# Performance work log

Hardware: AMD Instinct MI355X
Metric: run time of the kernel (lower is better)

The kernel has to match this reference:

```python
import jax, jax.numpy as jnp
import numpy as np

EPS = 1e-9


def _pairwise_sqdist(x1, x2):
    # x1: (B,n,3), x2: (B,m,3) -> (B,n,m) squared euclidean distances
    s1 = jnp.sum(x1 * x1, axis=-1)
    s2 = jnp.sum(x2 * x2, axis=-1)
    cross = jnp.einsum('bnd,bmd->bnm', x1, x2)
    return jnp.maximum(s1[:, :, None] + s2[:, None, :] - 2.0 * cross, 0.0)


def _approxmatch(x1, x2):
    # Faithful port of the approxmatch CUDA kernel (Fan et al. EMD approx).
    B, n, _ = x1.shape
    m = x2.shape[1]
    if n >= m:
        multiL, multiR = 1.0, float(n // m)   # integer division as in CUDA
    else:
        multiL, multiR = float(m // n), 1.0
    dist = _pairwise_sqdist(x1, x2)  # (B,n,m)
    # j = 7 .. -1 -> level = -4^j ; j = -2 -> level = 0  (10 sweeps total)
    levels = jnp.concatenate([
        -(4.0 ** jnp.arange(7, -2, -1, dtype=jnp.float32)),
        jnp.zeros((1,), jnp.float32)])
    match0 = jnp.zeros((B, n, m), jnp.float32)
    remainL0 = jnp.full((B, n), multiL, jnp.float32)
    remainR0 = jnp.full((B, m), multiR, jnp.float32)

    def body(carry, level):
        match, remainL, remainR = carry
        e = jnp.exp(level * dist)                              # (B,n,m)
        suml = EPS + jnp.einsum('bnm,bm->bn', e, remainR)
        ratioL = remainL / suml                                # (B,n)
        sumr = remainR * jnp.einsum('bnm,bn->bm', e, ratioL)   # (B,m)
        consumption = jnp.minimum(remainR / (sumr + EPS), 1.0)
        ratioR = consumption * remainR                         # (B,m)
        remainR = jnp.maximum(0.0, remainR - sumr)
        w = e * ratioL[:, :, None] * ratioR[:, None, :]        # flow k->l
        match = match + w
        remainL = jnp.maximum(0.0, remainL - jnp.sum(w, axis=-1))
        return (match, remainL, remainR), None

    (match, _, _), _ = jax.lax.scan(body, (match0, remainL0, remainR0), levels)
    return match, dist


def setup_inputs() -> dict:
    key = jax.random.key(0)
    k1, k2 = jax.random.split(key)
    B, N = 4, 4096
    xyz1 = jax.random.normal(k1, (B, 3, N), dtype=jnp.float32)
    xyz2 = jax.random.normal(k2, (B, 3, N), dtype=jnp.float32)
    return {"xyz1": xyz1, "xyz2": xyz2}


def reference(xyz1, xyz2):
    # transpose=True: BCN -> BNC
    x1 = jnp.transpose(xyz1, (0, 2, 1))
    x2 = jnp.transpose(xyz2, (0, 2, 1))
    match, dist = _approxmatch(x1, x2)
    d = jnp.sqrt(jnp.maximum(dist, 1e-20))
    cost = jnp.sum(match * d, axis=(1, 2))            # (B,)
    emd = cost / min(x1.shape[1], x2.shape[1])
    return jnp.mean(emd)                               # reduce_mean=True
```

## Files before the change

kernel.cpp:

```cpp
#include <hip/hip_runtime.h>


#define NPTS 4096
#define BATCH 4
#define EMD_EPS 1e-9f
#define TILE 1024
#define RPW 4
#define THREADS 256
#define RPB 16
#define NBLK (NPTS / RPB)

__device__ __forceinline__ float fexp2(float x) {
#if __has_builtin(__builtin_amdgcn_exp2f)
    return __builtin_amdgcn_exp2f(x);
#else
    return exp2f(x);
#endif
}
__device__ __forceinline__ float fsqrt(float x) {
#if __has_builtin(__builtin_amdgcn_sqrtf)
    return __builtin_amdgcn_sqrtf(x);
#else
    return __sqrtf(x);
#endif
}

__device__ __forceinline__ float wave_reduce(float v) {
    v += __shfl_xor(v, 32);
    v += __shfl_xor(v, 16);
    v += __shfl_xor(v, 8);
    v += __shfl_xor(v, 4);
    v += __shfl_xor(v, 2);
    v += __shfl_xor(v, 1);
    return v;
}

__global__ void k_init(float* __restrict__ remainL, float* __restrict__ remainR,
                       float* __restrict__ cost_part) {
    int i = blockIdx.x * blockDim.x + threadIdx.x;
    if (i < BATCH * NPTS) {
        remainL[i] = 1.0f;
        remainR[i] = 1.0f;
    }
    if (i < BATCH * NBLK) cost_part[i] = 0.0f;
}

__global__ __launch_bounds__(THREADS, 2) void k_ratioL0(
        const float* __restrict__ xyz1, const float* __restrict__ xyz2,
        float* __restrict__ ratioL, float ls2) {
    const int b = blockIdx.y;
    const int tid = threadIdx.x;
    const int wave = tid >> 6;
    const int lane = tid & 63;
    const int row0 = blockIdx.x * RPB + wave * RPW;

    const float* x1 = xyz1 + b * 3 * NPTS;
    const float* x2 = xyz2 + b * 3 * NPTS;
    const float2* x2x = (const float2*)(x2);
    const float2* x2y = (const float2*)(x2 + NPTS);
    const float2* x2z = (const float2*)(x2 + 2 * NPTS);

    float px[RPW], py[RPW], pz[RPW];
    float2 acc[RPW];
#pragma unroll
    for (int r = 0; r < RPW; ++r) {
        px[r] = x1[row0 + r];
        py[r] = x1[NPTS + row0 + r];
        pz[r] = x1[2 * NPTS + row0 + r];
        acc[r] = make_float2(0.0f, 0.0f);
    }
    __shared__ float4 sA[TILE / 2];
    __shared__ float2 sZ[TILE / 2];

    for (int c0 = 0; c0 < NPTS; c0 += TILE) {
        __syncthreads();
        for (int i = tid; i < TILE / 2; i += THREADS) {
            int e = c0 / 2 + i;
            float2 xx = x2x[e], yy = x2y[e];
            sA[i] = make_float4(xx.x, xx.y, yy.x, yy.y);
            sZ[i] = x2z[e];
        }
        __syncthreads();
#pragma unroll 2
        for (int j = 0; j < TILE / 128; ++j) {
            float4 a = sA[lane + 64 * j];
            float2 z = sZ[lane + 64 * j];
#pragma unroll
            for (int r = 0; r < RPW; ++r) {
                float dx0 = px[r] - a.x, dx1 = px[r] - a.y;
                float dy0 = py[r] - a.z, dy1 = py[r] - a.w;
                float dz0 = pz[r] - z.x, dz1 = pz[r] - z.y;
                float d0 = fmaf(dx0, dx0, fmaf(dy0, dy0, dz0 * dz0));
                float d1 = fmaf(dx1, dx1, fmaf(dy1, dy1, dz1 * dz1));
                acc[r].x += fexp2(ls2 * d0);
                acc[r].y += fexp2(ls2 * d1);
            }
        }
    }
#pragma unroll
    for (int r = 0; r < RPW; ++r) {
        float s = wave_reduce(acc[r].x + acc[r].y);
        if (lane == 0)
            ratioL[b * NPTS + row0 + r] = 1.0f / (EMD_EPS + s);
    }
}

__global__ __launch_bounds__(THREADS, 2) void k_ratioR(
        const float* __restrict__ xyz1, const float* __restrict__ xyz2,
        const float* __restrict__ ratioL, float* __restrict__ ratioR,
        float* __restrict__ remainR, float ls2) {
    const int b = blockIdx.y;
    const int tid = threadIdx.x;
    const int wave = tid >> 6;
    const int lane = tid & 63;
    const int col0 = blockIdx.x * RPB + wave * RPW;

    const float* x1 = xyz1 + b * 3 * NPTS;
    const float* x2 = xyz2 + b * 3 * NPTS;
    const float2* x1x = (const float2*)(x1);
    const float2* x1y = (const float2*)(x1 + NPTS);
    const float2* x1z = (const float2*)(x1 + 2 * NPTS);
    const float2* wLv = (const float2*)(ratioL + b * NPTS);

    float px[RPW], py[RPW], pz[RPW];
    float2 acc[RPW];
#pragma unroll
    for (int r = 0; r < RPW; ++r) {
        px[r] = x2[col0 + r];
        py[r] = x2[NPTS + col0 + r];
        pz[r] = x2[2 * NPTS + col0 + r];
        acc[r] = make_float2(0.0f, 0.0f);
    }
    __shared__ float4 sA[TILE / 2];
    __shared__ float4 sB[TILE / 2];

    for (int c0 = 0; c0 < NPTS; c0 += TILE) {
        __syncthreads();
        for (int i = tid; i < TILE / 2; i += THREADS) {
            int e = c0 / 2 + i;
            float2 xx = x1x[e], yy = x1y[e], zz = x1z[e], ww = wLv[e];
            sA[i] = make_float4(xx.x, xx.y, yy.x, yy.y);
            sB[i] = make_float4(zz.x, zz.y, ww.x, ww.y);
        }
        __syncthreads();
#pragma unroll 2
        for (int j = 0; j < TILE / 128; ++j) {
            float4 a = sA[lane + 64 * j];
            float4 bq = sB[lane + 64 * j];
#pragma unroll
            for (int r = 0; r < RPW; ++r) {
                float dx0 = px[r] - a.x, dx1 = px[r] - a.y;
                float dy0 = py[r] - a.z, dy1 = py[r] - a.w;
                float dz0 = pz[r] - bq.x, dz1 = pz[r] - bq.y;
                float d0 = fmaf(dx0, dx0, fmaf(dy0, dy0, dz0 * dz0));
                float d1 = fmaf(dx1, dx1, fmaf(dy1, dy1, dz1 * dz1));
                acc[r].x = fmaf(fexp2(ls2 * d0), bq.z, acc[r].x);
                acc[r].y = fmaf(fexp2(ls2 * d1), bq.w, acc[r].y);
            }
        }
    }
#pragma unroll
    for (int r = 0; r < RPW; ++r) {
        float s = wave_reduce(acc[r].x + acc[r].y);
        if (lane == 0) {
            int idx = b * NPTS + col0 + r;
            float rv = remainR[idx];
            float sumr = rv * s;
            float cons = fminf(rv / (sumr + EMD_EPS), 1.0f);
            ratioR[idx] = cons * rv;
            remainR[idx] = fmaxf(0.0f, rv - sumr);
        }
    }
}

template <bool SQ>
__global__ __launch_bounds__(THREADS, 2) void k_cost_fused(
        const float* __restrict__ xyz1, const float* __restrict__ xyz2,
        float* __restrict__ ratioL, const float* __restrict__ ratioR,
        float* __restrict__ remainL, const float* __restrict__ remainR,
        float* __restrict__ cost_part, float ls2, float ls2n) {
    const int b = blockIdx.y;
    const int tid = threadIdx.x;
    const int wave = tid >> 6;
    const int lane = tid & 63;
    const int row0 = blockIdx.x * RPB + wave * RPW;

    const float* x1 = xyz1 + b * 3 * NPTS;
    const float* x2 = xyz2 + b * 3 * NPTS;
    const float2* x2x = (const float2*)(x2);
    const float2* x2y = (const float2*)(x2 + NPTS);
    const float2* x2z = (const float2*)(x2 + 2 * NPTS);
    const float2* wRv = (const float2*)(ratioR + b * NPTS);
    const float2* w2v = (const float2*)(remainR + b * NPTS);

    float px[RPW], py[RPW], pz[RPW];
    float2 acc_a[RPW], acc_c[RPW], acc_s[RPW];
#pragma unroll
    for (int r = 0; r < RPW; ++r) {
        px[r] = x1[row0 + r];
        py[r] = x1[NPTS + row0 + r];
        pz[r] = x1[2 * NPTS + row0 + r];
        acc_a[r] = make_float2(0.0f, 0.0f);
        acc_c[r] = make_float2(0.0f, 0.0f);
        acc_s[r] = make_float2(0.0f, 0.0f);
    }
    __shared__ float4 sA[TILE / 2];
    __shared__ float4 sB[TILE / 2];
    __shared__ float2 sC[TILE / 2];
    __shared__ float s_cost[THREADS / 64];

    for (int c0 = 0; c0 < NPTS; c0 += TILE) {
        __syncthreads();
        for (int i = tid; i < TILE / 2; i += THREADS) {
            int e = c0 / 2 + i;
            float2 xx = x2x[e], yy = x2y[e], zz = x2z[e], wr = wRv[e];
            sA[i] = make_float4(xx.x, xx.y, yy.x, yy.y);
            sB[i] = make_float4(zz.x, zz.y, wr.x, wr.y);
            sC[i] = w2v[e];
        }
        __syncthreads();
#pragma unroll 2
        for (int j = 0; j < TILE / 128; ++j) {
            float4 a = sA[lane + 64 * j];
            float4 bq = sB[lane + 64 * j];
            float2 c = sC[lane + 64 * j];
#pragma unroll
            for (int r = 0; r < RPW; ++r) {
                float dx0 = px[r] - a.x, dx1 = px[r] - a.y;
                float dy0 = py[r] - a.z, dy1 = py[r] - a.w;
                float dz0 = pz[r] - bq.x, dz1 = pz[r] - bq.y;
                float d0 = fmaf(dx0, dx0, fmaf(dy0, dy0, dz0 * dz0));
                float d1 = fmaf(dx1, dx1, fmaf(dy1, dy1, dz1 * dz1));
                float er0, er1;
                if (SQ) {
                    float e20 = fexp2(ls2n * d0);
                    float e21 = fexp2(ls2n * d1);
                    acc_s[r].x = fmaf(e20, c.x, acc_s[r].x);
                    acc_s[r].y = fmaf(e21, c.y, acc_s[r].y);
                    float e40 = e20 * e20, e41 = e21 * e21;
                    er0 = (e40 * e40) * bq.z;
                    er1 = (e41 * e41) * bq.w;
                } else {
                    er0 = fexp2(ls2 * d0) * bq.z;
                    er1 = fexp2(ls2 * d1) * bq.w;
                    acc_s[r].x += c.x;
                    acc_s[r].y += c.y;
                }
                acc_a[r].x += er0;
                acc_a[r].y += er1;
                acc_c[r].x = fmaf(er0, fsqrt(d0), acc_c[r].x);
                acc_c[r].y = fmaf(er1, fsqrt(d1), acc_c[r].y);
            }
        }
    }
    float wcost = 0.0f;
#pragma unroll
    for (int r = 0; r < RPW; ++r) {
        float sa = wave_reduce(acc_a[r].x + acc_a[r].y);
        float sc = wave_reduce(acc_c[r].x + acc_c[r].y);
        float ss = wave_reduce(acc_s[r].x + acc_s[r].y);
        if (lane == 0) {
            int idx = b * NPTS + row0 + r;
            float rl = ratioL[idx];
            float rem = fmaxf(0.0f, remainL[idx] - rl * sa);
            remainL[idx] = rem;
            ratioL[idx] = rem / (EMD_EPS + ss);
            wcost = fmaf(rl, sc, wcost);
        }
    }
    if (lane == 0) s_cost[wave] = wcost;
    __syncthreads();
    if (tid == 0) {
        float t = s_cost[0] + s_cost[1] + s_cost[2] + s_cost[3];
        cost_part[b * NBLK + blockIdx.x] += t;
    }
}

__global__ void k_sum_ratioL(const float* __restrict__ ratioL, float* __restrict__ S_L) {
    const int b = blockIdx.x;
    const int tid = threadIdx.x;
    float s = 0.0f;
    for (int i = tid; i < NPTS; i += 256) s += ratioL[b * NPTS + i];
    s = wave_reduce(s);
    __shared__ float sw[4];
    if ((tid & 63) == 0) sw[tid >> 6] = s;
    __syncthreads();
    if (tid == 0) S_L[b] = sw[0] + sw[1] + sw[2] + sw[3];
}

__global__ void k_ratioR_l0(const float* __restrict__ remainR,
                            const float* __restrict__ S_L,
                            float* __restrict__ ratioR) {
    int i = blockIdx.x * blockDim.x + threadIdx.x;
    int b = i >> 12;
    float rv = remainR[i];
    float sumr = rv * S_L[b];
    float cons = fminf(rv / (sumr + EMD_EPS), 1.0f);
    ratioR[i] = cons * rv;
}

__global__ __launch_bounds__(THREADS, 2) void k_cost_l0(
        const float* __restrict__ xyz1, const float* __restrict__ xyz2,
        const float* __restrict__ ratioL, const float* __restrict__ ratioR,
        float* __restrict__ cost_part) {
    const int b = blockIdx.y;
    const int tid = threadIdx.x;
    const int wave = tid >> 6;
    const int lane = tid & 63;
    const int row0 = blockIdx.x * RPB + wave * RPW;

    const float* x1 = xyz1 + b * 3 * NPTS;
    const float* x2 = xyz2 + b * 3 * NPTS;
    const float2* x2x = (const float2*)(x2);
    const float2* x2y = (const float2*)(x2 + NPTS);
    const float2* x2z = (const float2*)(x2 + 2 * NPTS);
    const float2* wRv = (const float2*)(ratioR + b * NPTS);

    float px[RPW], py[RPW], pz[RPW];
    float2 acc_c[RPW];
#pragma unroll
    for (int r = 0; r < RPW; ++r) {
        px[r] = x1[row0 + r];
        py[r] = x1[NPTS + row0 + r];
        pz[r] = x1[2 * NPTS + row0 + r];
        acc_c[r] = make_float2(0.0f, 0.0f);
    }
    __shared__ float4 sA[TILE / 2];
    __shared__ float4 sB[TILE / 2];
    __shared__ float s_cost[THREADS / 64];

    for (int c0 = 0; c0 < NPTS; c0 += TILE) {
        __syncthreads();
        for (int i = tid; i < TILE / 2; i += THREADS) {
            int e = c0 / 2 + i;
            float2 xx = x2x[e], yy = x2y[e], zz = x2z[e], wr = wRv[e];
            sA[i] = make_float4(xx.x, xx.y, yy.x, yy.y);
            sB[i] = make_float4(zz.x, zz.y, wr.x, wr.y);
        }
        __syncthreads();
#pragma unroll 2
        for (int j = 0; j < TILE / 128; ++j) {
            float4 a = sA[lane + 64 * j];
            float4 bq = sB[lane + 64 * j];
#pragma unroll
            for (int r = 0; r < RPW; ++r) {
                float dx0 = px[r] - a.x, dx1 = px[r] - a.y;
                float dy0 = py[r] - a.z, dy1 = py[r] - a.w;
                float dz0 = pz[r] - bq.x, dz1 = pz[r] - bq.y;
                float d0 = fmaf(dx0, dx0, fmaf(dy0, dy0, dz0 * dz0));
                float d1 = fmaf(dx1, dx1, fmaf(dy1, dy1, dz1 * dz1));
                acc_c[r].x = fmaf(bq.z, fsqrt(d0), acc_c[r].x);
                acc_c[r].y = fmaf(bq.w, fsqrt(d1), acc_c[r].y);
            }
        }
    }
    float wcost = 0.0f;
#pragma unroll
    for (int r = 0; r < RPW; ++r) {
        float sc = wave_reduce(acc_c[r].x + acc_c[r].y);
        if (lane == 0)
            wcost = fmaf(ratioL[b * NPTS + row0 + r], sc, wcost);
    }
    if (lane == 0) s_cost[wave] = wcost;
    __syncthreads();
    if (tid == 0) {
        float t = s_cost[0] + s_cost[1] + s_cost[2] + s_cost[3];
        cost_part[b * NBLK + blockIdx.x] += t;
    }
}

__global__ void k_final(const float* __restrict__ cost_part, float* __restrict__ out) {
    const int tid = threadIdx.x;
    float s = 0.0f;
    for (int i = tid; i < BATCH * NBLK; i += 256) s += cost_part[i];
    s = wave_reduce(s);
    __shared__ float sw[4];
    if ((tid & 63) == 0) sw[tid >> 6] = s;
    __syncthreads();
    if (tid == 0) out[0] = (sw[0] + sw[1] + sw[2] + sw[3]) / ((float)NPTS * (float)BATCH);
}

extern "C" void kernel_launch(void* const* d_in, const int* in_sizes, int n_in,
                              void* d_out, int out_size, void* d_ws, size_t ws_size,
                              hipStream_t stream) {
    const float* xyz1 = (const float*)d_in[0];
    const float* xyz2 = (const float*)d_in[1];
    float* out = (float*)d_out;

    float* ws = (float*)d_ws;
    float* remainL  = ws;
    float* remainR  = ws + 1 * BATCH * NPTS;
    float* ratioL   = ws + 2 * BATCH * NPTS;
    float* ratioR   = ws + 3 * BATCH * NPTS;
    float* cost_part = ws + 4 * BATCH * NPTS;
    float* S_L      = cost_part + BATCH * NBLK;

    static const float levels[10] = {
        -16384.0f, -4096.0f, -1024.0f, -256.0f, -64.0f,
        -16.0f, -4.0f, -1.0f, -0.25f, 0.0f};
    float ls2[10];
    for (int t = 0; t < 10; ++t)
        ls2[t] = (float)(levels[t] * 1.4426950408889634);

    dim3 grid(NBLK, BATCH);

    k_init<<<(BATCH * NPTS + 255) / 256, 256, 0, stream>>>(remainL, remainR, cost_part);
    k_ratioL0<<<grid, THREADS, 0, stream>>>(xyz1, xyz2, ratioL, ls2[0]);
    for (int t = 0; t < 8; ++t) {
        k_ratioR<<<grid, THREADS, 0, stream>>>(xyz1, xyz2, ratioL, ratioR, remainR, ls2[t]);
        k_cost_fused<true><<<grid, THREADS, 0, stream>>>(xyz1, xyz2, ratioL, ratioR,
                                                         remainL, remainR, cost_part,
                                                         ls2[t], ls2[t + 1]);
    }
    k_ratioR<<<grid, THREADS, 0, stream>>>(xyz1, xyz2, ratioL, ratioR, remainR, ls2[8]);
    k_cost_fused<false><<<grid, THREADS, 0, stream>>>(xyz1, xyz2, ratioL, ratioR,
                                                      remainL, remainR, cost_part,
                                                      ls2[8], 0.0f);
    k_sum_ratioL<<<BATCH, 256, 0, stream>>>(ratioL, S_L);
    k_ratioR_l0<<<(BATCH * NPTS) / 256, 256, 0, stream>>>(remainR, S_L, ratioR);
    k_cost_l0<<<grid, THREADS, 0, stream>>>(xyz1, xyz2, ratioL, ratioR, cost_part);
    k_final<<<1, 256, 0, stream>>>(cost_part, out);
}
```

Measured before the change: 575.0 us.

## Halve rows per wave, raise occupancy, use packed float2 math, fold init kernels

```diff
diff --git a/kernel.cpp b/kernel.cpp
--- a/kernel.cpp
+++ b/kernel.cpp
@@ -5,10 +5,12 @@
 #define BATCH 4
 #define EMD_EPS 1e-9f
 #define TILE 1024
-#define RPW 4
+#define RPW 2
 #define THREADS 256
-#define RPB 16
+#define RPB 8
 #define NBLK (NPTS / RPB)
+
+typedef float v2f __attribute__((ext_vector_type(2)));
 
 __device__ __forceinline__ float fexp2(float x) {
 #if __has_builtin(__builtin_amdgcn_exp2f)
@@ -35,19 +37,10 @@
     return v;
 }
 
-__global__ void k_init(float* __restrict__ remainL, float* __restrict__ remainR,
-                       float* __restrict__ cost_part) {
-    int i = blockIdx.x * blockDim.x + threadIdx.x;
-    if (i < BATCH * NPTS) {
-        remainL[i] = 1.0f;
-        remainR[i] = 1.0f;
-    }
-    if (i < BATCH * NBLK) cost_part[i] = 0.0f;
-}
-
-__global__ __launch_bounds__(THREADS, 2) void k_ratioL0(
+__global__ __launch_bounds__(THREADS, 6) void k_ratioL0(
         const float* __restrict__ xyz1, const float* __restrict__ xyz2,
-        float* __restrict__ ratioL, float ls2) {
+        float* __restrict__ ratioL, float* __restrict__ remainL,
+        float* __restrict__ remainR, float ls2) {
     const int b = blockIdx.y;
     const int tid = threadIdx.x;
     const int wave = tid >> 6;
@@ -61,13 +54,13 @@
     const float2* x2z = (const float2*)(x2 + 2 * NPTS);
 
     float px[RPW], py[RPW], pz[RPW];
-    float2 acc[RPW];
+    v2f acc[RPW];
 #pragma unroll
     for (int r = 0; r < RPW; ++r) {
         px[r] = x1[row0 + r];
         py[r] = x1[NPTS + row0 + r];
         pz[r] = x1[2 * NPTS + row0 + r];
-        acc[r] = make_float2(0.0f, 0.0f);
+        acc[r] = (v2f)(0.0f);
     }
     __shared__ float4 sA[TILE / 2];
     __shared__ float2 sZ[TILE / 2];
@@ -85,27 +78,30 @@
         for (int j = 0; j < TILE / 128; ++j) {
             float4 a = sA[lane + 64 * j];
             float2 z = sZ[lane + 64 * j];
+            v2f ax = {a.x, a.y}, ay = {a.z, a.w}, az = {z.x, z.y};
 #pragma unroll
             for (int r = 0; r < RPW; ++r) {
-                float dx0 = px[r] - a.x, dx1 = px[r] - a.y;
-                float dy0 = py[r] - a.z, dy1 = py[r] - a.w;
-                float dz0 = pz[r] - z.x, dz1 = pz[r] - z.y;
-                float d0 = fmaf(dx0, dx0, fmaf(dy0, dy0, dz0 * dz0));
-                float d1 = fmaf(dx1, dx1, fmaf(dy1, dy1, dz1 * dz1));
-                acc[r].x += fexp2(ls2 * d0);
-                acc[r].y += fexp2(ls2 * d1);
+                v2f dx = px[r] - ax, dy = py[r] - ay, dz = pz[r] - az;
+                v2f d = dx * dx + dy * dy + dz * dz;
+                v2f sd = ls2 * d;
+                v2f e2 = {fexp2(sd.x), fexp2(sd.y)};
+                acc[r] += e2;
             }
         }
     }
 #pragma unroll
     for (int r = 0; r < RPW; ++r) {
         float s = wave_reduce(acc[r].x + acc[r].y);
-        if (lane == 0)
-            ratioL[b * NPTS + row0 + r] = 1.0f / (EMD_EPS + s);
-    }
-}
-
-__global__ __launch_bounds__(THREADS, 2) void k_ratioR(
+        if (lane == 0) {
+            int idx = b * NPTS + row0 + r;
+            ratioL[idx] = 1.0f / (EMD_EPS + s);
+            remainL[idx] = 1.0f;
+            remainR[idx] = 1.0f;
+        }
+    }
+}
+
+__global__ __launch_bounds__(THREADS, 6) void k_ratioR(
         const float* __restrict__ xyz1, const float* __restrict__ xyz2,
         const float* __restrict__ ratioL, float* __restrict__ ratioR,
         float* __restrict__ remainR, float ls2) {
@@ -123,13 +119,13 @@
     const float2* wLv = (const float2*)(ratioL + b * NPTS);
 
     float px[RPW], py[RPW], pz[RPW];
-    float2 acc[RPW];
+    v2f acc[RPW];
 #pragma unroll
     for (int r = 0; r < RPW; ++r) {
         px[r] = x2[col0 + r];
         py[r] = x2[NPTS + col0 + r];
         pz[r] = x2[2 * NPTS + col0 + r];
-        acc[r] = make_float2(0.0f, 0.0f);
+        acc[r] = (v2f)(0.0f);
     }
     __shared__ float4 sA[TILE / 2];
     __shared__ float4 sB[TILE / 2];
@@ -147,15 +143,15 @@
         for (int j = 0; j < TILE / 128; ++j) {
             float4 a = sA[lane + 64 * j];
             float4 bq = sB[lane + 64 * j];
+            v2f ax = {a.x, a.y}, ay = {a.z, a.w};
+            v2f az = {bq.x, bq.y}, aw = {bq.z, bq.w};
 #pragma unroll
             for (int r = 0; r < RPW; ++r) {
-                float dx0 = px[r] - a.x, dx1 = px[r] - a.y;
-                float dy0 = py[r] - a.z, dy1 = py[r] - a.w;
-                float dz0 = pz[r] - bq.x, dz1 = pz[r] - bq.y;
-                float d0 = fmaf(dx0, dx0, fmaf(dy0, dy0, dz0 * dz0));
-                float d1 = fmaf(dx1, dx1, fmaf(dy1, dy1, dz1 * dz1));
-                acc[r].x = fmaf(fexp2(ls2 * d0), bq.z, acc[r].x);
-                acc[r].y = fmaf(fexp2(ls2 * d1), bq.w, acc[r].y);
+                v2f dx = px[r] - ax, dy = py[r] - ay, dz = pz[r] - az;
+                v2f d = dx * dx + dy * dy + dz * dz;
+                v2f sd = ls2 * d;
+                v2f e2 = {fexp2(sd.x), fexp2(sd.y)};
+                acc[r] += e2 * aw;
             }
         }
     }
@@ -174,11 +170,11 @@
 }
 
 template <bool SQ>
-__global__ __launch_bounds__(THREADS, 2) void k_cost_fused(
+__global__ __launch_bounds__(THREADS, 6) void k_cost_fused(
         const float* __restrict__ xyz1, const float* __restrict__ xyz2,
         float* __restrict__ ratioL, const float* __restrict__ ratioR,
         float* __restrict__ remainL, const float* __restrict__ remainR,
-        float* __restrict__ cost_part, float ls2, float ls2n) {
+        float* __restrict__ cost_part, float ls2, float ls2n, int initCost) {
     const int b = blockIdx.y;
     const int tid = threadIdx.x;
     const int wave = tid >> 6;
@@ -194,15 +190,15 @@
     const float2* w2v = (const float2*)(remainR + b * NPTS);
 
     float px[RPW], py[RPW], pz[RPW];
-    float2 acc_a[RPW], acc_c[RPW], acc_s[RPW];
+    v2f acc_a[RPW], acc_c[RPW], acc_s[RPW];
 #pragma unroll
     for (int r = 0; r < RPW; ++r) {
         px[r] = x1[row0 + r];
         py[r] = x1[NPTS + row0 + r];
         pz[r] = x1[2 * NPTS + row0 + r];
-        acc_a[r] = make_float2(0.0f, 0.0f);
-        acc_c[r] = make_float2(0.0f, 0.0f);
-        acc_s[r] = make_float2(0.0f, 0.0f);
+        acc_a[r] = (v2f)(0.0f);
+        acc_c[r] = (v2f)(0.0f);
+        acc_s[r] = (v2f)(0.0f);
     }
     __shared__ float4 sA[TILE / 2];
     __shared__ float4 sB[TILE / 2];
@@ -224,32 +220,29 @@
             float4 a = sA[lane + 64 * j];
             float4 bq = sB[lane + 64 * j];
             float2 c = sC[lane + 64 * j];
+            v2f ax = {a.x, a.y}, ay = {a.z, a.w};
+            v2f az = {bq.x, bq.y}, wr = {bq.z, bq.w};
+            v2f cw = {c.x, c.y};
 #pragma unroll
             for (int r = 0; r < RPW; ++r) {
-                float dx0 = px[r] - a.x, dx1 = px[r] - a.y;
-                float dy0 = py[r] - a.z, dy1 = py[r] - a.w;
-                float dz0 = pz[r] - bq.x, dz1 = pz[r] - bq.y;
-                float d0 = fmaf(dx0, dx0, fmaf(dy0, dy0, dz0 * dz0));
-                float d1 = fmaf(dx1, dx1, fmaf(dy1, dy1, dz1 * dz1));
-                float er0, er1;
+                v2f dx = px[r] - ax, dy = py[r] - ay, dz = pz[r] - az;
+                v2f d = dx * dx + dy * dy + dz * dz;
+                v2f er;
                 if (SQ) {
-                    float e20 = fexp2(ls2n * d0);
-                    float e21 = fexp2(ls2n * d1);
-                    acc_s[r].x = fmaf(e20, c.x, acc_s[r].x);
-                    acc_s[r].y = fmaf(e21, c.y, acc_s[r].y);
-                    float e40 = e20 * e20, e41 = e21 * e21;
-                    er0 = (e40 * e40) * bq.z;
-                    er1 = (e41 * e41) * bq.w;
+                    v2f sd = ls2n * d;
+                    v2f e2 = {fexp2(sd.x), fexp2(sd.y)};
+                    acc_s[r] += e2 * cw;
+                    v2f e4 = e2 * e2;
+                    er = (e4 * e4) * wr;
                 } else {
-                    er0 = fexp2(ls2 * d0) * bq.z;
-                    er1 = fexp2(ls2 * d1) * bq.w;
-                    acc_s[r].x += c.x;
-                    acc_s[r].y += c.y;
+                    v2f sd = ls2 * d;
+                    v2f e1 = {fexp2(sd.x), fexp2(sd.y)};
+                    er = e1 * wr;
+                    acc_s[r] += cw;
                 }
-                acc_a[r].x += er0;
-                acc_a[r].y += er1;
-                acc_c[r].x = fmaf(er0, fsqrt(d0), acc_c[r].x);
-                acc_c[r].y = fmaf(er1, fsqrt(d1), acc_c[r].y);
+                acc_a[r] += er;
+                v2f sq = {fsqrt(d.x), fsqrt(d.y)};
+                acc_c[r] += er * sq;
             }
         }
     }
@@ -272,7 +265,8 @@
     __syncthreads();
     if (tid == 0) {
         float t = s_cost[0] + s_cost[1] + s_cost[2] + s_cost[3];
-        cost_part[b * NBLK + blockIdx.x] += t;
+        int ci = b * NBLK + blockIdx.x;
+        cost_part[ci] = (initCost ? t : cost_part[ci] + t);
     }
 }
 
@@ -288,42 +282,32 @@
     if (tid == 0) S_L[b] = sw[0] + sw[1] + sw[2] + sw[3];
 }
 
-__global__ void k_ratioR_l0(const float* __restrict__ remainR,
-                            const float* __restrict__ S_L,
-                            float* __restrict__ ratioR) {
-    int i = blockIdx.x * blockDim.x + threadIdx.x;
-    int b = i >> 12;
-    float rv = remainR[i];
-    float sumr = rv * S_L[b];
-    float cons = fminf(rv / (sumr + EMD_EPS), 1.0f);
-    ratioR[i] = cons * rv;
-}
-
-__global__ __launch_bounds__(THREADS, 2) void k_cost_l0(
+__global__ __launch_bounds__(THREADS, 6) void k_cost_l0(
         const float* __restrict__ xyz1, const float* __restrict__ xyz2,
-        const float* __restrict__ ratioL, const float* __restrict__ ratioR,
-        float* __restrict__ cost_part) {
+        const float* __restrict__ ratioL, const float* __restrict__ remainR,
+        const float* __restrict__ S_L, float* __restrict__ cost_part) {
     const int b = blockIdx.y;
     const int tid = threadIdx.x;
     const int wave = tid >> 6;
     const int lane = tid & 63;
     const int row0 = blockIdx.x * RPB + wave * RPW;
+    const float sL = S_L[b];
 
     const float* x1 = xyz1 + b * 3 * NPTS;
     const float* x2 = xyz2 + b * 3 * NPTS;
     const float2* x2x = (const float2*)(x2);
     const float2* x2y = (const float2*)(x2 + NPTS);
     const float2* x2z = (const float2*)(x2 + 2 * NPTS);
-    const float2* wRv = (const float2*)(ratioR + b * NPTS);
+    const float2* wRv = (const float2*)(remainR + b * NPTS);
 
     float px[RPW], py[RPW], pz[RPW];
-    float2 acc_c[RPW];
+    v2f acc_c[RPW];
 #pragma unroll
     for (int r = 0; r < RPW; ++r) {
         px[r] = x1[row0 + r];
         py[r] = x1[NPTS + row0 + r];
         pz[r] = x1[2 * NPTS + row0 + r];
-        acc_c[r] = make_float2(0.0f, 0.0f);
+        acc_c[r] = (v2f)(0.0f);
     }
     __shared__ float4 sA[TILE / 2];
     __shared__ float4 sB[TILE / 2];
@@ -333,24 +317,25 @@
         __syncthreads();
         for (int i = tid; i < TILE / 2; i += THREADS) {
             int e = c0 / 2 + i;
-            float2 xx = x2x[e], yy = x2y[e], zz = x2z[e], wr = wRv[e];
+            float2 xx = x2x[e], yy = x2y[e], zz = x2z[e], rv = wRv[e];
+            float wr0 = fminf(rv.x / (rv.x * sL + EMD_EPS), 1.0f) * rv.x;
+            float wr1 = fminf(rv.y / (rv.y * sL + EMD_EPS), 1.0f) * rv.y;
             sA[i] = make_float4(xx.x, xx.y, yy.x, yy.y);
-            sB[i] = make_float4(zz.x, zz.y, wr.x, wr.y);
+            sB[i] = make_float4(zz.x, zz.y, wr0, wr1);
         }
         __syncthreads();
 #pragma unroll 2
         for (int j = 0; j < TILE / 128; ++j) {
             float4 a = sA[lane + 64 * j];
             float4 bq = sB[lane + 64 * j];
+            v2f ax = {a.x, a.y}, ay = {a.z, a.w};
+            v2f az = {bq.x, bq.y}, wr = {bq.z, bq.w};
 #pragma unroll
             for (int r = 0; r < RPW; ++r) {
-                float dx0 = px[r] - a.x, dx1 = px[r] - a.y;
-                float dy0 = py[r] - a.z, dy1 = py[r] - a.w;
-                float dz0 = pz[r] - bq.x, dz1 = pz[r] - bq.y;
-                float d0 = fmaf(dx0, dx0, fmaf(dy0, dy0, dz0 * dz0));
-                float d1 = fmaf(dx1, dx1, fmaf(dy1, dy1, dz1 * dz1));
-                acc_c[r].x = fmaf(bq.z, fsqrt(d0), acc_c[r].x);
-                acc_c[r].y = fmaf(bq.w, fsqrt(d1), acc_c[r].y);
+                v2f dx = px[r] - ax, dy = py[r] - ay, dz = pz[r] - az;
+                v2f d = dx * dx + dy * dy + dz * dz;
+                v2f sq = {fsqrt(d.x), fsqrt(d.y)};
+                acc_c[r] += wr * sq;
             }
         }
     }
@@ -387,12 +372,13 @@
     const float* xyz2 = (const float*)d_in[1];
     float* out = (float*)d_out;
 
+    const int BN = BATCH * NPTS;
     float* ws = (float*)d_ws;
     float* remainL  = ws;
-    float* remainR  = ws + 1 * BATCH * NPTS;
-    float* ratioL   = ws + 2 * BATCH * NPTS;
-    float* ratioR   = ws + 3 * BATCH * NPTS;
-    float* cost_part = ws + 4 * BATCH * NPTS;
+    float* remainR  = ws + 1 * BN;
+    float* ratioL   = ws + 2 * BN;
+    float* ratioR   = ws + 3 * BN;
+    float* cost_part = ws + 4 * BN;
     float* S_L      = cost_part + BATCH * NBLK;
 
     static const float levels[10] = {
@@ -404,20 +390,18 @@
 
     dim3 grid(NBLK, BATCH);
 
-    k_init<<<(BATCH * NPTS + 255) / 256, 256, 0, stream>>>(remainL, remainR, cost_part);
-    k_ratioL0<<<grid, THREADS, 0, stream>>>(xyz1, xyz2, ratioL, ls2[0]);
+    k_ratioL0<<<grid, THREADS, 0, stream>>>(xyz1, xyz2, ratioL, remainL, remainR, ls2[0]);
     for (int t = 0; t < 8; ++t) {
         k_ratioR<<<grid, THREADS, 0, stream>>>(xyz1, xyz2, ratioL, ratioR, remainR, ls2[t]);
         k_cost_fused<true><<<grid, THREADS, 0, stream>>>(xyz1, xyz2, ratioL, ratioR,
                                                          remainL, remainR, cost_part,
-                                                         ls2[t], ls2[t + 1]);
+                                                         ls2[t], ls2[t + 1], t == 0 ? 1 : 0);
     }
     k_ratioR<<<grid, THREADS, 0, stream>>>(xyz1, xyz2, ratioL, ratioR, remainR, ls2[8]);
     k_cost_fused<false><<<grid, THREADS, 0, stream>>>(xyz1, xyz2, ratioL, ratioR,
                                                       remainL, remainR, cost_part,
-                                                      ls2[8], 0.0f);
+                                                      ls2[8], 0.0f, 0);
     k_sum_ratioL<<<BATCH, 256, 0, stream>>>(ratioL, S_L);
-    k_ratioR_l0<<<(BATCH * NPTS) / 256, 256, 0, stream>>>(remainR, S_L, ratioR);
-    k_cost_l0<<<grid, THREADS, 0, stream>>>(xyz1, xyz2, ratioL, ratioR, cost_part);
+    k_cost_l0<<<grid, THREADS, 0, stream>>>(xyz1, xyz2, ratioL, remainR, S_L, cost_part);
     k_final<<<1, 256, 0, stream>>>(cost_part, out);
 }
```

New measurement: 532.6 us. 1.08x faster.
